# Kernel optimization log

Measured on AMD Instinct MI355X. Metric: run time of the kernel, lower is better.

The kernel has to match this reference:

```python
import jax, jax.numpy as jnp
import numpy as np

B = 8192   # batch
S = 115    # state dim (fixed by slice layout)
E = 3072   # retrieval embed dim
C = 128    # compressed context dim
A = 23     # action dim
NE = 4096  # number of hyperedge keys
K = 10     # top-k retrieval
TAU = 1.0  # gumbel temperature
EPS = 1e-5 # layernorm eps


def _ln(x, g, b):
    m = x.mean(-1, keepdims=True)
    v = x.var(-1, keepdims=True)
    return (x - m) * jax.lax.rsqrt(v + EPS) * g + b


def _actor(ctx, extra, w1, b1, g1, be1, w2, b2, g2, be2, w3, b3):
    x = jnp.concatenate([ctx, extra], -1)
    x = jax.nn.relu(_ln(x @ w1 + b1, g1, be1))
    x = jax.nn.relu(_ln(x @ w2 + b2, g2, be2))
    return x @ w3 + b3


def setup_inputs() -> dict:
    key = jax.random.key(0)
    ks = iter(jax.random.split(key, 80))

    def W(shape):
        return jax.random.normal(next(ks), shape, jnp.float32) * (1.0 / float(np.sqrt(shape[0])))

    inp = {}
    inp["state"] = jax.random.normal(next(ks), (B, S), jnp.float32)
    u = jax.random.uniform(next(ks), (B, 4), jnp.float32, 1e-6, 1.0 - 1e-6)
    inp["gumbel_noise"] = -jnp.log(-jnp.log(u))  # standard Gumbel samples
    inp["keys"] = jax.random.normal(next(ks), (NE, E), jnp.float32)
    # state encoder 115 -> 512 -> 512 -> 3072 + LN
    inp["se_w1"] = W((S, 512)); inp["se_b1"] = jnp.zeros(512)
    inp["se_w2"] = W((512, 512)); inp["se_b2"] = jnp.zeros(512)
    inp["se_w3"] = W((512, E)); inp["se_b3"] = jnp.zeros(E)
    inp["se_g"] = jnp.ones(E); inp["se_beta"] = jnp.zeros(E)
    # context compressor 3072 -> 512 -> 128 + LN
    inp["cc_w1"] = W((E, 512)); inp["cc_b1"] = jnp.zeros(512)
    inp["cc_w2"] = W((512, C)); inp["cc_b2"] = jnp.zeros(C)
    inp["cc_g"] = jnp.ones(C); inp["cc_beta"] = jnp.zeros(C)
    # 4 actor experts, differing only in extra-slice width
    for p, e in [("a_pre", 50), ("a_scene", 20), ("a_effect", 10), ("a_rule", 15)]:
        inp[p + "_w1"] = W((C + e, C)); inp[p + "_b1"] = jnp.zeros(C)
        inp[p + "_g1"] = jnp.ones(C); inp[p + "_be1"] = jnp.zeros(C)
        inp[p + "_w2"] = W((C, C)); inp[p + "_b2"] = jnp.zeros(C)
        inp[p + "_g2"] = jnp.ones(C); inp[p + "_be2"] = jnp.zeros(C)
        inp[p + "_w3"] = W((C, A)) * 0.01; inp[p + "_b3"] = jnp.zeros(A)  # orthogonal gain=0.01 approx
    # gumbel router 115 -> 64 -> 64 -> 4
    inp["r_w1"] = W((S, 64)); inp["r_b1"] = jnp.zeros(64)
    inp["r_w2"] = W((64, 64)); inp["r_b2"] = jnp.zeros(64)
    inp["r_w3"] = W((64, 4)); inp["r_b3"] = jnp.zeros(4)
    # critic 115 -> 256 -> 256 -> 1
    inp["c_w1"] = W((S, 256)); inp["c_b1"] = jnp.zeros(256)
    inp["c_w2"] = W((256, 256)); inp["c_b2"] = jnp.zeros(256)
    inp["c_w3"] = W((256, 1)); inp["c_b3"] = jnp.zeros(1)
    return inp


def reference(state, gumbel_noise, keys, se_w1, se_b1, se_w2, se_b2, se_w3, se_b3, se_g, se_beta, cc_w1, cc_b1, cc_w2, cc_b2, cc_g, cc_beta, a_pre_w1, a_pre_b1, a_pre_g1, a_pre_be1, a_pre_w2, a_pre_b2, a_pre_g2, a_pre_be2, a_pre_w3, a_pre_b3, a_scene_w1, a_scene_b1, a_scene_g1, a_scene_be1, a_scene_w2, a_scene_b2, a_scene_g2, a_scene_be2, a_scene_w3, a_scene_b3, a_effect_w1, a_effect_b1, a_effect_g1, a_effect_be1, a_effect_w2, a_effect_b2, a_effect_g2, a_effect_be2, a_effect_w3, a_effect_b3, a_rule_w1, a_rule_b1, a_rule_g1, a_rule_be1, a_rule_w2, a_rule_b2, a_rule_g2, a_rule_be2, a_rule_w3, a_rule_b3, r_w1, r_b1, r_w2, r_b2, r_w3, r_b3, c_w1, c_b1, c_w2, c_b2, c_w3, c_b3):
    # 1) state -> query (StateEncoder)
    q = jax.nn.relu(state @ se_w1 + se_b1)
    q = jax.nn.relu(q @ se_w2 + se_b2)
    q = _ln(q @ se_w3 + se_b3, se_g, se_beta)  # (B, E)
    # 2) top-k hard retrieval from hypergraph memory (cosine sim)
    qn = q * jax.lax.rsqrt(jnp.sum(q * q, -1, keepdims=True) + 1e-12)
    kn = keys * jax.lax.rsqrt(jnp.sum(keys * keys, -1, keepdims=True) + 1e-12)
    scores = qn @ kn.T                          # (B, NE)
    _, idx = jax.lax.top_k(scores, K)           # (B, K)
    context = jnp.take(keys, idx, axis=0).mean(1)  # (B, E) mean-pool top-k raw embeddings
    # 3) compress to shared knowledge
    h = jax.nn.relu(context @ cc_w1 + cc_b1)
    shared = _ln(h @ cc_w2 + cc_b2, cc_g, cc_beta)  # (B, C)
    # 4) state slices + 4 actor experts
    belief = state[:, :50]
    location = state[:, 20:40]
    hp = state[:, 40:50]
    inv = state[:, 45:60]
    lp = _actor(shared, belief, a_pre_w1, a_pre_b1, a_pre_g1, a_pre_be1, a_pre_w2, a_pre_b2, a_pre_g2, a_pre_be2, a_pre_w3, a_pre_b3)
    ls = _actor(shared, location, a_scene_w1, a_scene_b1, a_scene_g1, a_scene_be1, a_scene_w2, a_scene_b2, a_scene_g2, a_scene_be2, a_scene_w3, a_scene_b3)
    le = _actor(shared, hp, a_effect_w1, a_effect_b1, a_effect_g1, a_effect_be1, a_effect_w2, a_effect_b2, a_effect_g2, a_effect_be2, a_effect_w3, a_effect_b3)
    lr = _actor(shared, inv, a_rule_w1, a_rule_b1, a_rule_g1, a_rule_be1, a_rule_w2, a_rule_b2, a_rule_g2, a_rule_be2, a_rule_w3, a_rule_b3)
    # 5) gumbel-softmax hard router (straight-through)
    rh = jax.nn.relu(state @ r_w1 + r_b1)
    rh = jax.nn.relu(rh @ r_w2 + r_b2)
    rl = jnp.clip(rh @ r_w3 + r_b3, -20.0, 20.0)
    y_soft = jax.nn.softmax((rl + gumbel_noise) / TAU, -1)
    y_hard = jax.nn.one_hot(jnp.argmax(y_soft, -1), 4, dtype=y_soft.dtype)
    alpha = y_soft + jax.lax.stop_gradient(y_hard - y_soft)  # (B, 4)
    # 6) combine expert logits
    all_l = jnp.stack([lp, ls, le, lr], 1)      # (B, 4, A)
    logits = jnp.einsum('bk,bka->ba', alpha, all_l)
    # critic value
    v = jax.nn.relu(state @ c_w1 + c_b1)
    v = jax.nn.relu(v @ c_w2 + c_b2)
    value = v @ c_w3 + c_b3                      # (B, 1)
    return (logits, alpha, value)
```

## Files before the change

kernel.cpp:

```cpp
#include <hip/hip_runtime.h>

constexpr int Bz = 8192;
constexpr int Sz = 115;
constexpr int Ez = 3072;
constexpr int NEz = 4096;

typedef __attribute__((ext_vector_type(8))) short short8;
typedef __attribute__((ext_vector_type(4))) float floatx4;
typedef unsigned short ushort_t;
typedef unsigned int uint_t;

__device__ __forceinline__ ushort_t f2bf(float f) {
  uint_t u = __float_as_uint(f);
  uint_t r = (u + 0x7FFFu + ((u >> 16) & 1u)) >> 16;
  return (ushort_t)r;
}
__device__ __forceinline__ float bf2f(ushort_t b) {
  uint_t u = ((uint_t)b) << 16;
  return __uint_as_float(u);
}
__device__ __forceinline__ ushort_t f2key(float v) {
  _Float16 h = (_Float16)v;
  ushort_t b = __builtin_bit_cast(ushort_t, h);
  return b ^ ((b & 0x8000u) ? 0xFFFFu : 0x8000u);
}
__device__ __forceinline__ uint_t umax_(uint_t a, uint_t b) { return a > b ? a : b; }

__device__ __forceinline__ void gload16(const ushort_t* g, ushort_t* l) {
  __builtin_amdgcn_global_load_lds(
      (__attribute__((address_space(1))) const void*)g,
      (__attribute__((address_space(3))) void*)l, 16, 0, 0);
}

template<bool RELU, bool BIAS>
__global__ __launch_bounds__(256)
void gemm128(const float* __restrict__ A, const float* __restrict__ Bm,
             const float* __restrict__ bias, float* __restrict__ C,
             int N, int Kd)
{
  __shared__ float As[16][132];
  __shared__ float Bs[16][132];
  const int t  = threadIdx.x;
  const int tx = t & 15, ty = t >> 4;
  const int row0 = blockIdx.y * 128;
  const int col0 = blockIdx.x * 128;
  const int ar = t >> 2, ac = (t & 3) * 4;
  const int bk = t >> 5, bc = (t & 31) * 4;
  const bool a4 = (Kd & 3) == 0;

  float acc[8][8];
#pragma unroll
  for (int i = 0; i < 8; ++i)
#pragma unroll
    for (int j = 0; j < 8; ++j) acc[i][j] = 0.f;

  for (int k0 = 0; k0 < Kd; k0 += 16) {
    const bool fullA = (k0 + 16 <= Kd) && a4;
    {
      const float* ap = A + (size_t)(row0 + ar) * Kd + k0 + ac;
      if (fullA) {
        float4 v0 = *(const float4*)ap;
        float4 v1 = *(const float4*)(ap + (size_t)64 * Kd);
        As[ac + 0][ar] = v0.x; As[ac + 1][ar] = v0.y;
        As[ac + 2][ar] = v0.z; As[ac + 3][ar] = v0.w;
        As[ac + 0][ar + 64] = v1.x; As[ac + 1][ar + 64] = v1.y;
        As[ac + 2][ar + 64] = v1.z; As[ac + 3][ar + 64] = v1.w;
      } else {
#pragma unroll
        for (int e = 0; e < 4; ++e) {
          const int k = k0 + ac + e;
          float v0 = 0.f, v1 = 0.f;
          if (k < Kd) { v0 = ap[e]; v1 = ap[e + (size_t)64 * Kd]; }
          As[ac + e][ar] = v0; As[ac + e][ar + 64] = v1;
        }
      }
    }
    {
      const float* bp = Bm + (size_t)(k0 + bk) * N + col0 + bc;
      if (k0 + 16 <= Kd) {
        *(float4*)&Bs[bk][bc]     = *(const float4*)bp;
        *(float4*)&Bs[bk + 8][bc] = *(const float4*)(bp + (size_t)8 * N);
      } else {
        float4 z; z.x = z.y = z.z = z.w = 0.f;
        *(float4*)&Bs[bk][bc]     = (k0 + bk     < Kd) ? *(const float4*)bp : z;
        *(float4*)&Bs[bk + 8][bc] = (k0 + bk + 8 < Kd) ? *(const float4*)(bp + (size_t)8 * N) : z;
      }
    }
    __syncthreads();
#pragma unroll
    for (int kk = 0; kk < 16; ++kk) {
      float a[8], b[8];
      *(float4*)&a[0] = *(const float4*)&As[kk][ty * 4];
      *(float4*)&a[4] = *(const float4*)&As[kk][64 + ty * 4];
      *(float4*)&b[0] = *(const float4*)&Bs[kk][tx * 4];
      *(float4*)&b[4] = *(const float4*)&Bs[kk][64 + tx * 4];
#pragma unroll
      for (int i = 0; i < 8; ++i)
#pragma unroll
        for (int j = 0; j < 8; ++j)
          acc[i][j] = fmaf(a[i], b[j], acc[i][j]);
    }
    __syncthreads();
  }

  float bv[8];
#pragma unroll
  for (int j = 0; j < 8; ++j) bv[j] = 0.f;
  if (BIAS) {
    *(float4*)&bv[0] = *(const float4*)&bias[col0 + tx * 4];
    *(float4*)&bv[4] = *(const float4*)&bias[col0 + 64 + tx * 4];
  }
#pragma unroll
  for (int i = 0; i < 8; ++i) {
    const int r = row0 + ((i < 4) ? (ty * 4 + i) : (64 + ty * 4 + i - 4));
    float o[8];
#pragma unroll
    for (int j = 0; j < 8; ++j) {
      o[j] = acc[i][j] + bv[j];
      if (RELU) o[j] = fmaxf(o[j], 0.f);
    }
    *(float4*)&C[(size_t)r * N + col0 + tx * 4]      = *(float4*)&o[0];
    *(float4*)&C[(size_t)r * N + col0 + 64 + tx * 4] = *(float4*)&o[4];
  }
}

struct GPart {
  const float* A; const float* Bm; const float* bias;
  float* C; ushort_t* Ch; ushort_t* Cl;
  int N; int Kd; int nbx;
};

__global__ __launch_bounds__(256)
void gemm128_dual(GPart g0, GPart g1)
{
  __shared__ float As[16][132];
  __shared__ float Bs[16][132];
  const int t  = threadIdx.x;
  const int tx = t & 15, ty = t >> 4;
  const bool p0 = (int)blockIdx.x < g0.nbx;
  GPart g = p0 ? g0 : g1;
  const int bx = p0 ? blockIdx.x : (blockIdx.x - g0.nbx);
  const int row0 = blockIdx.y * 128;
  const int col0 = bx * 128;
  const int Kd = g.Kd, N = g.N;
  const int ar = t >> 2, ac = (t & 3) * 4;
  const int bk = t >> 5, bc = (t & 31) * 4;
  const bool a4 = (Kd & 3) == 0;

  float acc[8][8];
#pragma unroll
  for (int i = 0; i < 8; ++i)
#pragma unroll
    for (int j = 0; j < 8; ++j) acc[i][j] = 0.f;

  for (int k0 = 0; k0 < Kd; k0 += 16) {
    const bool fullA = (k0 + 16 <= Kd) && a4;
    {
      const float* ap = g.A + (size_t)(row0 + ar) * Kd + k0 + ac;
      if (fullA) {
        float4 v0 = *(const float4*)ap;
        float4 v1 = *(const float4*)(ap + (size_t)64 * Kd);
        As[ac + 0][ar] = v0.x; As[ac + 1][ar] = v0.y;
        As[ac + 2][ar] = v0.z; As[ac + 3][ar] = v0.w;
        As[ac + 0][ar + 64] = v1.x; As[ac + 1][ar + 64] = v1.y;
        As[ac + 2][ar + 64] = v1.z; As[ac + 3][ar + 64] = v1.w;
      } else {
#pragma unroll
        for (int e = 0; e < 4; ++e) {
          const int k = k0 + ac + e;
          float v0 = 0.f, v1 = 0.f;
          if (k < Kd) { v0 = ap[e]; v1 = ap[e + (size_t)64 * Kd]; }
          As[ac + e][ar] = v0; As[ac + e][ar + 64] = v1;
        }
      }
    }
    {
      const float* bp = g.Bm + (size_t)(k0 + bk) * N + col0 + bc;
      if (k0 + 16 <= Kd) {
        *(float4*)&Bs[bk][bc]     = *(const float4*)bp;
        *(float4*)&Bs[bk + 8][bc] = *(const float4*)(bp + (size_t)8 * N);
      } else {
        float4 z; z.x = z.y = z.z = z.w = 0.f;
        *(float4*)&Bs[bk][bc]     = (k0 + bk     < Kd) ? *(const float4*)bp : z;
        *(float4*)&Bs[bk + 8][bc] = (k0 + bk + 8 < Kd) ? *(const float4*)(bp + (size_t)8 * N) : z;
      }
    }
    __syncthreads();
#pragma unroll
    for (int kk = 0; kk < 16; ++kk) {
      float a[8], b[8];
      *(float4*)&a[0] = *(const float4*)&As[kk][ty * 4];
      *(float4*)&a[4] = *(const float4*)&As[kk][64 + ty * 4];
      *(float4*)&b[0] = *(const float4*)&Bs[kk][tx * 4];
      *(float4*)&b[4] = *(const float4*)&Bs[kk][64 + tx * 4];
#pragma unroll
      for (int i = 0; i < 8; ++i)
#pragma unroll
        for (int j = 0; j < 8; ++j)
          acc[i][j] = fmaf(a[i], b[j], acc[i][j]);
    }
    __syncthreads();
  }

  float bv[8];
  *(float4*)&bv[0] = *(const float4*)&g.bias[col0 + tx * 4];
  *(float4*)&bv[4] = *(const float4*)&g.bias[col0 + 64 + tx * 4];
#pragma unroll
  for (int i = 0; i < 8; ++i) {
    const int r = row0 + ((i < 4) ? (ty * 4 + i) : (64 + ty * 4 + i - 4));
    float o[8];
#pragma unroll
    for (int j = 0; j < 8; ++j) o[j] = fmaxf(acc[i][j] + bv[j], 0.f);
    const size_t i0 = (size_t)r * N + col0 + tx * 4;
    const size_t i1 = i0 + 64;
    if (g.C) {
      *(float4*)&g.C[i0] = *(float4*)&o[0];
      *(float4*)&g.C[i1] = *(float4*)&o[4];
    }
    if (g.Ch) {
      ushort4 h0, l0, h1, l1;
      h0.x = f2bf(o[0]); l0.x = f2bf(o[0] - bf2f(h0.x));
      h0.y = f2bf(o[1]); l0.y = f2bf(o[1] - bf2f(h0.y));
      h0.z = f2bf(o[2]); l0.z = f2bf(o[2] - bf2f(h0.z));
      h0.w = f2bf(o[3]); l0.w = f2bf(o[3] - bf2f(h0.w));
      h1.x = f2bf(o[4]); l1.x = f2bf(o[4] - bf2f(h1.x));
      h1.y = f2bf(o[5]); l1.y = f2bf(o[5] - bf2f(h1.y));
      h1.z = f2bf(o[6]); l1.z = f2bf(o[6] - bf2f(h1.z));
      h1.w = f2bf(o[7]); l1.w = f2bf(o[7] - bf2f(h1.w));
      *(ushort4*)&g.Ch[i0] = h0; *(ushort4*)&g.Cl[i0] = l0;
      *(ushort4*)&g.Ch[i1] = h1; *(ushort4*)&g.Cl[i1] = l1;
    }
  }
}

__global__ __launch_bounds__(512, 2)
void screen256(const ushort_t* __restrict__ A, const ushort_t* __restrict__ B,
               ushort_t* __restrict__ Cout, int N, int Kd)
{
  __shared__ ushort_t AL[2 * 256 * 64];
  __shared__ ushort_t BL[2 * 256 * 64];
  const int t = threadIdx.x;
  const int lane = t & 63;
  const int wid = t >> 6;
  const int wr = wid >> 2;
  const int wc = wid & 3;
  const int mr = lane & 15, qd = lane >> 4;

  const int lin = (int)blockIdx.y * 16 + (int)blockIdx.x;
  const int xcd = lin & 7, cid = lin >> 3;
  const int bxs = xcd * 2 + (cid >> 5);
  const int bys = cid & 31;
  const int row0 = bys << 8;
  const int col0 = bxs << 8;
  const int NT = Kd >> 6;

  const int l8 = lane >> 3;
  const int c8 = (lane & 7) ^ l8;
  const ushort_t* pA = A + (size_t)(row0 + wr * 128 + wc * 16 + l8) * Kd + c8 * 8;
  const ushort_t* pB = B + (size_t)(col0 + (wid >> 1) * 64 + (wid & 1) * 16 + l8) * Kd + c8 * 8;
  ushort_t* aWp = &AL[wr * 8192 + wc * 1024];
  ushort_t* bWp = &BL[(wid >> 1) * 4096 + (wid & 1) * 1024];

  const int swz = (mr & 7) << 4;
  const int aRow = (wr * 128 + mr) * 64;
  const int bRow = (wc * 64 + mr) * 64;
  const int cu0 = ((qd * 16) ^ swz) >> 1;
  const int cu1 = ((64 + qd * 16) ^ swz) >> 1;

  floatx4 acc[8][4];
#pragma unroll
  for (int i = 0; i < 8; ++i)
#pragma unroll
    for (int j = 0; j < 4; ++j) acc[i][j] = (floatx4){0.f, 0.f, 0.f, 0.f};

  short8 aF[4][2], b01[2][2], b23[2][2];

#define STA(db, h, tile) do {                                            \
    const int kt_ = ((tile) < NT ? (tile) : 0) << 6;                     \
    gload16(pA + (size_t)((h) * 64) * Kd + kt_,                          \
            aWp + (db) * 16384 + (h) * 4096);                            \
    gload16(pA + (size_t)((h) * 64 + 8) * Kd + kt_,                      \
            aWp + (db) * 16384 + (h) * 4096 + 512);                      \
  } while (0)
#define STB(db, g, tile) do {                                            \
    const int kt_ = ((tile) < NT ? (tile) : 0) << 6;                     \
    gload16(pB + (size_t)((g) * 32) * Kd + kt_,                          \
            bWp + (db) * 16384 + (g) * 2048);                            \
    gload16(pB + (size_t)((g) * 32 + 8) * Kd + kt_,                      \
            bWp + (db) * 16384 + (g) * 2048 + 512);                      \
  } while (0)
#define LDA(db, half)                                                    \
  _Pragma("unroll")                                                      \
  for (int i_ = 0; i_ < 4; ++i_) {                                       \
    const int b_ = (db) * 16384 + aRow + ((half) * 4 + i_) * 1024;       \
    aF[i_][0] = *(const short8*)&AL[b_ + cu0];                           \
    aF[i_][1] = *(const short8*)&AL[b_ + cu1];                           \
  }
#define LDB(db, jh, bF)                                                  \
  _Pragma("unroll")                                                      \
  for (int j_ = 0; j_ < 2; ++j_) {                                       \
    const int b_ = (db) * 16384 + bRow + ((jh) * 2 + j_) * 1024;         \
    bF[j_][0] = *(const short8*)&BL[b_ + cu0];                           \
    bF[j_][1] = *(const short8*)&BL[b_ + cu1];                           \
  }
#define MM(ih, jh, bF)                                                   \
  _Pragma("unroll")                                                      \
  for (int s_ = 0; s_ < 2; ++s_)                                         \
    _Pragma("unroll")                                                    \
    for (int i_ = 0; i_ < 4; ++i_)                                       \
      _Pragma("unroll")                                                  \
      for (int j_ = 0; j_ < 2; ++j_)                                     \
        acc[(ih)*4+i_][(jh)*2+j_] = __builtin_amdgcn_mfma_f32_16x16x32_bf16( \
            aF[i_][s_], bF[j_][s_], acc[(ih)*4+i_][(jh)*2+j_], 0, 0, 0);
#define SCH0() __builtin_amdgcn_sched_barrier(0)
#define BARM() do { __builtin_amdgcn_s_barrier();                        \
                    asm volatile("" ::: "memory"); } while (0)
#define WLG()  do { asm volatile("s_waitcnt lgkmcnt(0)" ::: "memory");   \
                    SCH0(); } while (0)
#define WVM(n) asm volatile("s_waitcnt vmcnt(" #n ")" ::: "memory")

  STA(0, 0, 0); STB(0, 1, 0); STA(0, 1, 0); STB(0, 0, 0);
  WVM(4);
  STA(1, 0, 1); STB(1, 1, 1); STA(1, 1, 1);
  WVM(6);
  BARM();

  for (int it = 0; it < NT / 2; ++it) {
    const int tp = it * 2;
    LDA(0, 0); LDB(0, 0, b01);
    STB(1, 0, tp + 1);
    __builtin_amdgcn_s_barrier(); WLG();
    __builtin_amdgcn_s_setprio(1); MM(0, 0, b01); __builtin_amdgcn_s_setprio(0);
    BARM();
    LDB(0, 1, b23);
    STA(0, 0, tp + 2);
    __builtin_amdgcn_s_barrier(); WLG();
    __builtin_amdgcn_s_setprio(1); MM(0, 1, b23); __builtin_amdgcn_s_setprio(0);
    BARM();
    LDA(0, 1);
    STB(0, 1, tp + 2);
    __builtin_amdgcn_s_barrier(); WLG();
    __builtin_amdgcn_s_setprio(1); MM(1, 1, b23); __builtin_amdgcn_s_setprio(0);
    BARM();
    LDB(0, 0, b01);
    STA(0, 1, tp + 2);
    WVM(6);
    __builtin_amdgcn_s_barrier(); WLG();
    __builtin_amdgcn_s_setprio(1); MM(1, 0, b01); __builtin_amdgcn_s_setprio(0);
    BARM();
    LDA(1, 0); LDB(1, 0, b01);
    STB(0, 0, tp + 2);
    __builtin_amdgcn_s_barrier(); WLG();
    __builtin_amdgcn_s_setprio(1); MM(0, 0, b01); __builtin_amdgcn_s_setprio(0);
    BARM();
    LDB(1, 1, b23);
    STA(1, 0, tp + 3);
    __builtin_amdgcn_s_barrier(); WLG();
    __builtin_amdgcn_s_setprio(1); MM(0, 1, b23); __builtin_amdgcn_s_setprio(0);
    BARM();
    LDA(1, 1);
    STB(1, 1, tp + 3);
    __builtin_amdgcn_s_barrier(); WLG();
    __builtin_amdgcn_s_setprio(1); MM(1, 1, b23); __builtin_amdgcn_s_setprio(0);
    BARM();
    LDB(1, 0, b01);
    STA(1, 1, tp + 3);
    WVM(6);
    __builtin_amdgcn_s_barrier(); WLG();
    __builtin_amdgcn_s_setprio(1); MM(1, 0, b01); __builtin_amdgcn_s_setprio(0);
    BARM();
  }

  asm volatile("s_waitcnt vmcnt(0) lgkmcnt(0)" ::: "memory");
  __syncthreads();

#undef STA
#undef STB
#undef LDA
#undef LDB
#undef MM
#undef SCH0
#undef BARM
#undef WLG
#undef WVM

#pragma unroll
  for (int i = 0; i < 8; ++i) {
#pragma unroll
    for (int j = 0; j < 4; ++j) {
      const int col = col0 + wc * 64 + j * 16 + mr;
#pragma unroll
      for (int r = 0; r < 4; ++r) {
        const int row = row0 + wr * 128 + i * 16 + qd * 4 + r;
        Cout[(size_t)row * N + col] = f2key(acc[i][j][r]);
      }
    }
  }
}

template<int EPI>
__global__ __launch_bounds__(256)
void mfma3_bt(const ushort_t* __restrict__ Ah, const ushort_t* __restrict__ Alo,
              const ushort_t* __restrict__ Bh, const ushort_t* __restrict__ Blo,
              const float* __restrict__ bias, float* __restrict__ Cout,
              ushort_t* __restrict__ Ch, ushort_t* __restrict__ Cl,
              int N, int Kd)
{
  __shared__ ushort_t AhL[128 * 32];
  __shared__ ushort_t AlL[128 * 32];
  __shared__ ushort_t BhL[128 * 32];
  __shared__ ushort_t BlL[128 * 32];
  const int t = threadIdx.x;
  const int wid = t >> 6, lane = t & 63;
  const int wr = wid >> 1, wc = wid & 1;
  const int row0 = blockIdx.y * 128;
  const int col0 = blockIdx.x * 128;
  const int srow = lane >> 2;
  const int scol = (lane & 3) * 8;

  const size_t aoff0 = (size_t)(row0 + wid * 16 + srow) * Kd + scol;
  const size_t aoff1 = (size_t)(row0 + (wid + 4) * 16 + srow) * Kd + scol;
  const size_t boff0 = (size_t)(col0 + wid * 16 + srow) * Kd + scol;
  const size_t boff1 = (size_t)(col0 + (wid + 4) * 16 + srow) * Kd + scol;
  const int l0 = (wid * 16) * 32;
  const int l1 = ((wid + 4) * 16) * 32;

  const int mr = lane & 15, qd = lane >> 4;

  floatx4 acc[4][4];
#pragma unroll
  for (int i = 0; i < 4; ++i)
#pragma unroll
    for (int j = 0; j < 4; ++j) acc[i][j] = (floatx4){0.f, 0.f, 0.f, 0.f};

  for (int kb = 0; kb < Kd; kb += 32) {
    gload16(Ah + aoff0 + kb, &AhL[l0]);
    gload16(Ah + aoff1 + kb, &AhL[l1]);
    gload16(Alo + aoff0 + kb, &AlL[l0]);
    gload16(Alo + aoff1 + kb, &AlL[l1]);
    gload16(Bh + boff0 + kb, &BhL[l0]);
    gload16(Bh + boff1 + kb, &BhL[l1]);
    gload16(Blo + boff0 + kb, &BlL[l0]);
    gload16(Blo + boff1 + kb, &BlL[l1]);
    __syncthreads();
    short8 ahF[4], alF[4], bhF[4], blF[4];
#pragma unroll
    for (int i = 0; i < 4; ++i) {
      const int o = (wr * 64 + i * 16 + mr) * 32 + qd * 8;
      ahF[i] = *(const short8*)&AhL[o];
      alF[i] = *(const short8*)&AlL[o];
    }
#pragma unroll
    for (int j = 0; j < 4; ++j) {
      const int o = (wc * 64 + j * 16 + mr) * 32 + qd * 8;
      bhF[j] = *(const short8*)&BhL[o];
      blF[j] = *(const short8*)&BlL[o];
    }
#pragma unroll
    for (int i = 0; i < 4; ++i)
#pragma unroll
      for (int j = 0; j < 4; ++j) {
        acc[i][j] = __builtin_amdgcn_mfma_f32_16x16x32_bf16(alF[i], bhF[j], acc[i][j], 0, 0, 0);
        acc[i][j] = __builtin_amdgcn_mfma_f32_16x16x32_bf16(ahF[i], blF[j], acc[i][j], 0, 0, 0);
        acc[i][j] = __builtin_amdgcn_mfma_f32_16x16x32_bf16(ahF[i], bhF[j], acc[i][j], 0, 0, 0);
      }
    __syncthreads();
  }

#pragma unroll
  for (int i = 0; i < 4; ++i) {
#pragma unroll
    for (int j = 0; j < 4; ++j) {
      const int col = col0 + wc * 64 + j * 16 + mr;
#pragma unroll
      for (int r = 0; r < 4; ++r) {
        const int row = row0 + wr * 64 + i * 16 + qd * 4 + r;
        const float v = acc[i][j][r] + bias[col];
        if (EPI == 0) {
          Cout[(size_t)row * N + col] = v;
        } else {
          const float y = fmaxf(v, 0.f);
          const ushort_t h = f2bf(y);
          Ch[(size_t)row * N + col] = h;
          Cl[(size_t)row * N + col] = f2bf(y - bf2f(h));
        }
      }
    }
  }
}

__global__ __launch_bounds__(256)
void mfma_bt64(const ushort_t* __restrict__ A, const ushort_t* __restrict__ B,
               const float* __restrict__ bias, float* __restrict__ Cout,
               int N, int Kd)
{
  __shared__ ushort_t Al[2 * 64 * 32];
  __shared__ ushort_t Bl[2 * 128 * 32];
  const int t = threadIdx.x;
  const int wid = t >> 6, lane = t & 63;
  const int row0 = blockIdx.y << 6;
  const int col0 = blockIdx.x << 7;
  const int srow = lane >> 2;
  const int scol = (lane & 3) * 8;
  const int mr = lane & 15, qd = lane >> 4;

  const ushort_t* gsrc[6];
  ushort_t* ldst[6];
#pragma unroll
  for (int m = 0; m < 6; ++m) {
    const int c = wid * 6 + m;
    if (c < 8) {
      const int sub = c >> 2, grp = c & 3;
      gsrc[m] = A + (size_t)(row0 + grp * 16 + srow) * Kd + sub * 32 + scol;
      ldst[m] = &Al[sub * 2048 + (grp * 16 + srow) * 32];
    } else {
      const int b = c - 8, sub = b >> 3, grp = b & 7;
      gsrc[m] = B + (size_t)(col0 + grp * 16 + srow) * Kd + sub * 32 + scol;
      ldst[m] = &Bl[sub * 4096 + (grp * 16 + srow) * 32];
    }
  }

  floatx4 acc[4][2];
#pragma unroll
  for (int i = 0; i < 4; ++i)
#pragma unroll
    for (int j = 0; j < 2; ++j) acc[i][j] = (floatx4){0.f, 0.f, 0.f, 0.f};

  for (int kb = 0; kb < Kd; kb += 64) {
#pragma unroll
    for (int m = 0; m < 6; ++m) gload16(gsrc[m] + kb, ldst[m]);
    __syncthreads();
#pragma unroll
    for (int sub = 0; sub < 2; ++sub) {
      short8 aF[4], bF[2];
#pragma unroll
      for (int i = 0; i < 4; ++i)
        aF[i] = *(const short8*)&Al[sub * 2048 + (i * 16 + mr) * 32 + qd * 8];
#pragma unroll
      for (int j = 0; j < 2; ++j)
        bF[j] = *(const short8*)&Bl[sub * 4096 + (wid * 32 + j * 16 + mr) * 32 + qd * 8];
#pragma unroll
      for (int i = 0; i < 4; ++i)
#pragma unroll
        for (int j = 0; j < 2; ++j)
          acc[i][j] = __builtin_amdgcn_mfma_f32_16x16x32_bf16(aF[i], bF[j], acc[i][j], 0, 0, 0);
    }
    __syncthreads();
  }

#pragma unroll
  for (int i = 0; i < 4; ++i) {
#pragma unroll
    for (int j = 0; j < 2; ++j) {
      const int col = col0 + wid * 32 + j * 16 + mr;
#pragma unroll
      for (int r = 0; r < 4; ++r) {
        const int row = row0 + i * 16 + qd * 4 + r;
        Cout[(size_t)row * N + col] = fmaxf(acc[i][j][r] + bias[col], 0.f);
      }
    }
  }
}

__global__ __launch_bounds__(256)
void gemm_scores(const float* __restrict__ A, const float* __restrict__ Bm,
                 const float* __restrict__ rk, ushort_t* __restrict__ S)
{
  __shared__ float As[16][132];
  __shared__ float Bs[16][132];
  const int t  = threadIdx.x;
  const int tx = t & 15, ty = t >> 4;
  const int row0 = blockIdx.y * 128;
  const int col0 = blockIdx.x * 128;
  const int ar = t >> 2, ac = (t & 3) * 4;
  const int Kd = Ez;

  float acc[8][8];
#pragma unroll
  for (int i = 0; i < 8; ++i)
#pragma unroll
    for (int j = 0; j < 8; ++j) acc[i][j] = 0.f;

  for (int k0 = 0; k0 < Kd; k0 += 16) {
    {
      const float* ap = A + (size_t)(row0 + ar) * Kd + k0 + ac;
      float4 v0 = *(const float4*)ap;
      float4 v1 = *(const float4*)(ap + (size_t)64 * Kd);
      As[ac + 0][ar] = v0.x; As[ac + 1][ar] = v0.y;
      As[ac + 2][ar] = v0.z; As[ac + 3][ar] = v0.w;
      As[ac + 0][ar + 64] = v1.x; As[ac + 1][ar + 64] = v1.y;
      As[ac + 2][ar + 64] = v1.z; As[ac + 3][ar + 64] = v1.w;
    }
    {
      const float* bp = Bm + (size_t)(col0 + ar) * Kd + k0 + ac;
      float4 v0 = *(const float4*)bp;
      float4 v1 = *(const float4*)(bp + (size_t)64 * Kd);
      Bs[ac + 0][ar] = v0.x; Bs[ac + 1][ar] = v0.y;
      Bs[ac + 2][ar] = v0.z; Bs[ac + 3][ar] = v0.w;
      Bs[ac + 0][ar + 64] = v1.x; Bs[ac + 1][ar + 64] = v1.y;
      Bs[ac + 2][ar + 64] = v1.z; Bs[ac + 3][ar + 64] = v1.w;
    }
    __syncthreads();
#pragma unroll
    for (int kk = 0; kk < 16; ++kk) {
      float a[8], b[8];
      *(float4*)&a[0] = *(const float4*)&As[kk][ty * 4];
      *(float4*)&a[4] = *(const float4*)&As[kk][64 + ty * 4];
      *(float4*)&b[0] = *(const float4*)&Bs[kk][tx * 4];
      *(float4*)&b[4] = *(const float4*)&Bs[kk][64 + tx * 4];
#pragma unroll
      for (int i = 0; i < 8; ++i)
#pragma unroll
        for (int j = 0; j < 8; ++j)
          acc[i][j] = fmaf(a[i], b[j], acc[i][j]);
    }
    __syncthreads();
  }

  float rk0[8];
  *(float4*)&rk0[0] = *(const float4*)&rk[col0 + tx * 4];
  *(float4*)&rk0[4] = *(const float4*)&rk[col0 + 64 + tx * 4];
#pragma unroll
  for (int i = 0; i < 8; ++i) {
    const int r = row0 + ((i < 4) ? (ty * 4 + i) : (64 + ty * 4 + i - 4));
    ushort4 h0, h1;
    h0.x = f2key(acc[i][0] * rk0[0]); h0.y = f2key(acc[i][1] * rk0[1]);
    h0.z = f2key(acc[i][2] * rk0[2]); h0.w = f2key(acc[i][3] * rk0[3]);
    h1.x = f2key(acc[i][4] * rk0[4]); h1.y = f2key(acc[i][5] * rk0[5]);
    h1.z = f2key(acc[i][6] * rk0[6]); h1.w = f2key(acc[i][7] * rk0[7]);
    *(ushort4*)&S[(size_t)r * NEz + col0 + tx * 4]      = h0;
    *(ushort4*)&S[(size_t)r * NEz + col0 + 64 + tx * 4] = h1;
  }
}

struct LN4 {
  const float* W[4]; const float* b[4]; const float* g[4]; const float* be[4];
  int eoff[4]; int elen[4];
};

template<bool RELU, bool HASEXT>
__global__ __launch_bounds__(256)
void gemm_ln4(const float* __restrict__ A1base, size_t a1stride, int K1,
              const float* __restrict__ A2, LN4 p,
              float* __restrict__ outbase, size_t ostride)
{
  __shared__ float As[32][68];
  __shared__ float Bs[32][132];
  __shared__ float rsum[64][17];
  __shared__ float rsq[64][17];
  __shared__ float stm[64], str[64];
  const int a = blockIdx.y;
  const float* A1 = A1base + (size_t)a * a1stride;
  float* out = outbase + (size_t)a * ostride;
  const float* W = p.W[a];
  const float* bias = p.b[a];
  const float* g = p.g[a];
  const float* be = p.be[a];
  const int eoff = HASEXT ? p.eoff[a] : 0;
  const int K2 = HASEXT ? p.elen[a] : 0;

  const int t = threadIdx.x;
  const int tx = t & 15, ty = t >> 4;
  const int row0 = blockIdx.x * 64;
  const int Kt = K1 + K2;
  const int ar = t >> 2, ac = (t & 3) * 8;
  const int bk = t >> 3, bc = (t & 7) * 16;

  float acc[4][8];
#pragma unroll
  for (int i = 0; i < 4; ++i)
#pragma unroll
    for (int j = 0; j < 8; ++j) acc[i][j] = 0.f;

  for (int k0 = 0; k0 < Kt; k0 += 32) {
    const int grow = row0 + ar;
#pragma unroll
    for (int e = 0; e < 8; ++e) {
      const int k = k0 + ac + e;
      float v = 0.f;
      if (k < K1)      v = A1[(size_t)grow * K1 + k];
      else if (k < Kt) v = A2[(size_t)grow * 115 + eoff + (k - K1)];
      As[ac + e][ar] = v;
    }
    {
      const int k = k0 + bk;
#pragma unroll
      for (int qd = 0; qd < 4; ++qd) {
// ... 639 lines not shown
```

Before: 1.306 ms.

## Double-buffer MFMA fragments in screen256 and drop XCD block remapping

Rewrites the screen256 main loop so the LDS reads of the next A/B fragment quarter are issued right after each MFMA batch, into separate register sets. This lets LDS reads overlap with the next matrix-core phase instead of waiting before it. It also reorders the global-to-LDS staging and removes the XCD-aware block index swizzle, going back to a plain blockIdx mapping. The extra fragment registers may raise register pressure at 2 blocks/CU, and dropping the swizzle may reduce L2 locality across XCDs.

```diff
diff --git a/kernel.cpp b/kernel.cpp
--- a/kernel.cpp
+++ b/kernel.cpp
@@ -245,13 +245,8 @@
   const int wr = wid >> 2;
   const int wc = wid & 3;
   const int mr = lane & 15, qd = lane >> 4;
-
-  const int lin = (int)blockIdx.y * 16 + (int)blockIdx.x;
-  const int xcd = lin & 7, cid = lin >> 3;
-  const int bxs = xcd * 2 + (cid >> 5);
-  const int bys = cid & 31;
-  const int row0 = bys << 8;
-  const int col0 = bxs << 8;
+  const int row0 = (int)blockIdx.y << 8;
+  const int col0 = (int)blockIdx.x << 8;
   const int NT = Kd >> 6;
 
   const int l8 = lane >> 3;
@@ -273,7 +268,7 @@
 #pragma unroll
     for (int j = 0; j < 4; ++j) acc[i][j] = (floatx4){0.f, 0.f, 0.f, 0.f};
 
-  short8 aF[4][2], b01[2][2], b23[2][2];
+  short8 A0r[4][2], A1r[4][2], B0r[2][2], B1r[2][2];
 
 #define STA(db, h, tile) do {                                            \
     const int kt_ = ((tile) < NT ? (tile) : 0) << 6;                     \
@@ -289,21 +284,21 @@
     gload16(pB + (size_t)((g) * 32 + 8) * Kd + kt_,                      \
             bWp + (db) * 16384 + (g) * 2048 + 512);                      \
   } while (0)
-#define LDA(db, half)                                                    \
+#define LDAm(dst, db, half)                                              \
   _Pragma("unroll")                                                      \
   for (int i_ = 0; i_ < 4; ++i_) {                                       \
     const int b_ = (db) * 16384 + aRow + ((half) * 4 + i_) * 1024;       \
-    aF[i_][0] = *(const short8*)&AL[b_ + cu0];                           \
-    aF[i_][1] = *(const short8*)&AL[b_ + cu1];                           \
-  }
-#define LDB(db, jh, bF)                                                  \
+    dst[i_][0] = *(const short8*)&AL[b_ + cu0];                          \
+    dst[i_][1] = *(const short8*)&AL[b_ + cu1];                          \
+  }
+#define LDBm(dst, db, jh)                                                \
   _Pragma("unroll")                                                      \
   for (int j_ = 0; j_ < 2; ++j_) {                                       \
     const int b_ = (db) * 16384 + bRow + ((jh) * 2 + j_) * 1024;         \
-    bF[j_][0] = *(const short8*)&BL[b_ + cu0];                           \
-    bF[j_][1] = *(const short8*)&BL[b_ + cu1];                           \
-  }
-#define MM(ih, jh, bF)                                                   \
+    dst[j_][0] = *(const short8*)&BL[b_ + cu0];                          \
+    dst[j_][1] = *(const short8*)&BL[b_ + cu1];                          \
+  }
+#define MMq(ih, jh, As_, Bs_)                                            \
   _Pragma("unroll")                                                      \
   for (int s_ = 0; s_ < 2; ++s_)                                         \
     _Pragma("unroll")                                                    \
@@ -311,63 +306,62 @@
       _Pragma("unroll")                                                  \
       for (int j_ = 0; j_ < 2; ++j_)                                     \
         acc[(ih)*4+i_][(jh)*2+j_] = __builtin_amdgcn_mfma_f32_16x16x32_bf16( \
-            aF[i_][s_], bF[j_][s_], acc[(ih)*4+i_][(jh)*2+j_], 0, 0, 0);
-#define SCH0() __builtin_amdgcn_sched_barrier(0)
+            As_[i_][s_], Bs_[j_][s_], acc[(ih)*4+i_][(jh)*2+j_], 0, 0, 0);
 #define BARM() do { __builtin_amdgcn_s_barrier();                        \
                     asm volatile("" ::: "memory"); } while (0)
 #define WLG()  do { asm volatile("s_waitcnt lgkmcnt(0)" ::: "memory");   \
-                    SCH0(); } while (0)
+                    __builtin_amdgcn_sched_barrier(0); } while (0)
 #define WVM(n) asm volatile("s_waitcnt vmcnt(" #n ")" ::: "memory")
-
-  STA(0, 0, 0); STB(0, 1, 0); STA(0, 1, 0); STB(0, 0, 0);
-  WVM(4);
-  STA(1, 0, 1); STB(1, 1, 1); STA(1, 1, 1);
-  WVM(6);
+#define PRIO1() __builtin_amdgcn_s_setprio(1)
+#define PRIO0() __builtin_amdgcn_s_setprio(0)
+
+  STA(0, 0, 0); STB(0, 0, 0); STB(0, 1, 0); STA(0, 1, 0);
+  STA(1, 0, 1); STB(1, 0, 1); STB(1, 1, 1); STA(1, 1, 1);
+  WVM(8);
+  LDAm(A0r, 0, 0); LDBm(B0r, 0, 0);
   BARM();
 
   for (int it = 0; it < NT / 2; ++it) {
     const int tp = it * 2;
-    LDA(0, 0); LDB(0, 0, b01);
-    STB(1, 0, tp + 1);
     __builtin_amdgcn_s_barrier(); WLG();
-    __builtin_amdgcn_s_setprio(1); MM(0, 0, b01); __builtin_amdgcn_s_setprio(0);
+    PRIO1(); MMq(0, 0, A0r, B0r); PRIO0();
+    LDBm(B1r, 0, 1);
     BARM();
-    LDB(0, 1, b23);
-    STA(0, 0, tp + 2);
+    STA(0, 0, tp + 2); STB(0, 0, tp + 2);
     __builtin_amdgcn_s_barrier(); WLG();
-    __builtin_amdgcn_s_setprio(1); MM(0, 1, b23); __builtin_amdgcn_s_setprio(0);
+    PRIO1(); MMq(0, 1, A0r, B1r); PRIO0();
+    LDAm(A1r, 0, 1);
     BARM();
-    LDA(0, 1);
     STB(0, 1, tp + 2);
-    __builtin_amdgcn_s_barrier(); WLG();
-    __builtin_amdgcn_s_setprio(1); MM(1, 1, b23); __builtin_amdgcn_s_setprio(0);
-    BARM();
-    LDB(0, 0, b01);
-    STA(0, 1, tp + 2);
     WVM(6);
     __builtin_amdgcn_s_barrier(); WLG();
-    __builtin_amdgcn_s_setprio(1); MM(1, 0, b01); __builtin_amdgcn_s_setprio(0);
+    PRIO1(); MMq(1, 1, A1r, B1r); PRIO0();
+    LDAm(A0r, 1, 0);
     BARM();
-    LDA(1, 0); LDB(1, 0, b01);
-    STB(0, 0, tp + 2);
+    STA(0, 1, tp + 2);
     __builtin_amdgcn_s_barrier(); WLG();
-    __builtin_amdgcn_s_setprio(1); MM(0, 0, b01); __builtin_amdgcn_s_setprio(0);
+    PRIO1(); MMq(1, 0, A1r, B0r); PRIO0();
+    LDBm(B1r, 1, 0);
     BARM();
-    LDB(1, 1, b23);
-    STA(1, 0, tp + 3);
     __builtin_amdgcn_s_barrier(); WLG();
-    __builtin_amdgcn_s_setprio(1); MM(0, 1, b23); __builtin_amdgcn_s_setprio(0);
+    PRIO1(); MMq(0, 0, A0r, B1r); PRIO0();
+    LDBm(B0r, 1, 1);
     BARM();
-    LDA(1, 1);
+    STA(1, 0, tp + 3); STB(1, 0, tp + 3);
+    __builtin_amdgcn_s_barrier(); WLG();
+    PRIO1(); MMq(0, 1, A0r, B0r); PRIO0();
+    LDAm(A1r, 1, 1);
+    BARM();
     STB(1, 1, tp + 3);
-    __builtin_amdgcn_s_barrier(); WLG();
-    __builtin_amdgcn_s_setprio(1); MM(1, 1, b23); __builtin_amdgcn_s_setprio(0);
-    BARM();
-    LDB(1, 0, b01);
-    STA(1, 1, tp + 3);
     WVM(6);
     __builtin_amdgcn_s_barrier(); WLG();
-    __builtin_amdgcn_s_setprio(1); MM(1, 0, b01); __builtin_amdgcn_s_setprio(0);
+    PRIO1(); MMq(1, 1, A1r, B0r); PRIO0();
+    LDAm(A0r, 0, 0);
+    BARM();
+    STA(1, 1, tp + 3);
+    __builtin_amdgcn_s_barrier(); WLG();
+    PRIO1(); MMq(1, 0, A1r, B1r); PRIO0();
+    LDBm(B0r, 0, 0);
     BARM();
   }
 
@@ -376,13 +370,14 @@
 
 #undef STA
 #undef STB
-#undef LDA
-#undef LDB
-#undef MM
-#undef SCH0
+#undef LDAm
+#undef LDBm
+#undef MMq
 #undef BARM
 #undef WLG
 #undef WVM
+#undef PRIO1
+#undef PRIO0
 
 #pragma unroll
   for (int i = 0; i < 8; ++i) {
```

Result: faster. 1.263 ms (-3.4%).
